# Kernel tuning notes

Measured on AMD Instinct MI355X. Metric: run time of the kernel, lower is better.

## Reference

```python
import jax, jax.numpy as jnp
import numpy as np

B, T, C = 2, 2048, 1024
E, F = 8, 1024        # n_experts, expert ffn dim
FS = 2048             # shared expert ffn dim
TOP_K = 2


def setup_inputs() -> dict:
    key = jax.random.key(0)
    ks = jax.random.split(key, 6)
    s = lambda *d: 1.0 / np.sqrt(d[-1])
    return {
        "hidden_tensor": jax.random.normal(ks[0], (B, T, C), jnp.float32),
        "w_router": jax.random.normal(ks[1], (E, C), jnp.float32) * s(C),
        "w1_stack": jax.random.normal(ks[2], (E, F, C), jnp.float32) * s(C),
        "w2_stack": jax.random.normal(ks[3], (E, C, F), jnp.float32) * s(F),
        "ws1": jax.random.normal(ks[4], (FS, C), jnp.float32) * s(C),
        "ws2": jax.random.normal(ks[5], (C, FS), jnp.float32) * s(FS),
    }


def reference(hidden_tensor, w_router, w1_stack, w2_stack, ws1, ws2):
    Bb, Tt, Cc = hidden_tensor.shape
    x = hidden_tensor.reshape(-1, Cc)                      # (t, C)
    t = x.shape[0]

    # --- router: softmax over experts, top-k, renormalize ---
    logits = x @ w_router.T                                # (t, E)
    probs = jax.nn.softmax(logits, axis=-1)
    expert_weight, expert_idx = jax.lax.top_k(probs, TOP_K)  # (t, k)
    expert_weight = expert_weight / jnp.sum(expert_weight, axis=-1, keepdims=True)

    # --- dispatch: stable sort token-expert pairs by expert id ---
    flat_e = expert_idx.reshape(-1)                        # (t*k,)
    order = jnp.argsort(flat_e, stable=True)
    sorted_e = flat_e[order]
    flat_tok = jnp.repeat(jnp.arange(t), TOP_K)
    sorted_tok = flat_tok[order]
    sorted_w = expert_weight.reshape(-1)[order]

    counts = jnp.bincount(sorted_e, length=E)              # (E,)
    offsets = jnp.concatenate([jnp.zeros((1,), counts.dtype), jnp.cumsum(counts)])
    local_pos = jnp.arange(t * TOP_K) - offsets[sorted_e]  # position within expert bin

    cap = t * TOP_K  # static capacity (>= true cnt_max), padding rows stay zero
    binned = jnp.zeros((E, cap, Cc), x.dtype).at[sorted_e, local_pos].set(x[sorted_tok])

    # --- grouped expert FFN with squared-ReLU ---
    inter = jnp.einsum('ecd,efd->ecf', binned, w1_stack)   # (E, cap, F)
    inter = jnp.square(jax.nn.relu(inter))
    outb = jnp.einsum('ecf,edf->ecd', inter, w2_stack)     # (E, cap, C)

    # --- combine: gather back, weight, scatter-add to tokens ---
    flat_out = outb[sorted_e, local_pos] * sorted_w[:, None]
    moe_out = jnp.zeros((t, Cc), x.dtype).at[sorted_tok].add(flat_out)
    moe_out = moe_out.reshape(Bb, Tt, Cc)

    # --- shared expert on residual (squared-ReLU MLP) ---
    sh = jnp.square(jax.nn.relu(jnp.einsum('btc,fc->btf', hidden_tensor, ws1)))
    shared_out = jnp.einsum('btf,cf->btc', sh, ws2)

    return shared_out + moe_out
```

## Files before the change

### kernel.cpp

```cpp
#include <hip/hip_runtime.h>
#include <math.h>

typedef unsigned short u16;
typedef unsigned int u32;

typedef __attribute__((ext_vector_type(8))) short bf16x8;
typedef __attribute__((ext_vector_type(4))) float f32x4;

__device__ __forceinline__ u16 f2bf(float f) {
  union { float f; u32 u; } v; v.f = f;
  u32 r = v.u + 0x7FFFu + ((v.u >> 16) & 1u);
  return (u16)(r >> 16);
}
__device__ __forceinline__ float bf2f(u16 h) {
  union { u32 u; float f; } v; v.u = ((u32)h) << 16; return v.f;
}

typedef const u32 __attribute__((address_space(1)))* gas1_t;
typedef u32 __attribute__((address_space(3)))* las3_t;

__device__ __forceinline__ void gload16(const void* g, void* l) {
  __builtin_amdgcn_global_load_lds((gas1_t)g, (las3_t)l, 16, 0, 0);
}

struct Tile { int kind; int g0; int n0; int e; };

__global__ __launch_bounds__(256) void prep_kernel(
    const float* __restrict__ x, const float* __restrict__ wr,
    u16* __restrict__ xb, int* __restrict__ tokE, float* __restrict__ tokW,
    const float4* __restrict__ w1, const float4* __restrict__ w2,
    const float4* __restrict__ s1, const float4* __restrict__ s2,
    ushort4* __restrict__ o1, ushort4* __restrict__ o2,
    ushort4* __restrict__ o3, ushort4* __restrict__ o4) {
  if (blockIdx.x >= 1024) {
    size_t i = (size_t)(blockIdx.x - 1024) * 256 + threadIdx.x;
    const size_t n1 = 2097152, n2 = 2097152, n3 = 524288;
    float4 v; ushort4* o; size_t j;
    if (i < n1)              { v = w1[i];            o = o1; j = i; }
    else if (i < n1+n2)      { v = w2[i-n1];         o = o2; j = i-n1; }
    else if (i < n1+n2+n3)   { v = s1[i-n1-n2];      o = o3; j = i-n1-n2; }
    else                     { v = s2[i-n1-n2-n3];   o = o4; j = i-n1-n2-n3; }
    ushort4 r; r.x = f2bf(v.x); r.y = f2bf(v.y); r.z = f2bf(v.z); r.w = f2bf(v.w);
    o[j] = r;
    return;
  }
  const int wv = threadIdx.x >> 6, lane = threadIdx.x & 63;
  const int tok = blockIdx.x * 4 + wv;
  const float4* xp = (const float4*)(x + (size_t)tok * 1024);
  float4 xv[4];
#pragma unroll
  for (int i = 0; i < 4; ++i) xv[i] = xp[i * 64 + lane];
  ushort4* xo = (ushort4*)xb + (size_t)tok * 256;
#pragma unroll
  for (int i = 0; i < 4; ++i) {
    ushort4 o;
    o.x = f2bf(xv[i].x); o.y = f2bf(xv[i].y); o.z = f2bf(xv[i].z); o.w = f2bf(xv[i].w);
    xo[i * 64 + lane] = o;
  }
  float acc[8];
#pragma unroll
  for (int e = 0; e < 8; ++e) acc[e] = 0.f;
#pragma unroll
  for (int e = 0; e < 8; ++e) {
    const float4* wp = (const float4*)(wr + e * 1024);
#pragma unroll
    for (int i = 0; i < 4; ++i) {
      float4 w4 = wp[i * 64 + lane];
      acc[e] += xv[i].x * w4.x + xv[i].y * w4.y + xv[i].z * w4.z + xv[i].w * w4.w;
    }
  }
#pragma unroll
  for (int m = 32; m > 0; m >>= 1)
#pragma unroll
    for (int e = 0; e < 8; ++e) acc[e] += __shfl_xor(acc[e], m, 64);
  if (lane == 0) {
    int e0 = 0;
#pragma unroll
    for (int e = 1; e < 8; ++e) if (acc[e] > acc[e0]) e0 = e;
    int e1 = (e0 == 0) ? 1 : 0;
#pragma unroll
    for (int e = 0; e < 8; ++e) if (e != e0 && acc[e] > acc[e1]) e1 = e;
    float p1 = __expf(acc[e1] - acc[e0]);
    float w1_ = p1 / (1.f + p1);
    float w0 = 1.f - w1_;
    tokE[tok * 2] = e0; tokE[tok * 2 + 1] = e1;
    tokW[tok * 2] = w0; tokW[tok * 2 + 1] = w1_;
  }
}

__global__ __launch_bounds__(256) void plan_kernel(
    const int* __restrict__ tokE, const float* __restrict__ tokW,
    Tile* __restrict__ upT, Tile* __restrict__ downT,
    int* __restrict__ rowtok, float* __restrict__ roww, int* __restrict__ invrow) {
  const int t = threadIdx.x, lane = t & 63, wv = t >> 6;
  int myE[32];
#pragma unroll
  for (int i = 0; i < 32; ++i) myE[i] = tokE[t * 32 + i];
  int lcnt[8] = {};
#pragma unroll
  for (int i = 0; i < 32; ++i) ++lcnt[myE[i]];

  __shared__ int wtot[8][4];
  __shared__ int aoffS[9];
  __shared__ int etile[72 * 2];
  int excl[8];
#pragma unroll
  for (int e = 0; e < 8; ++e) {
    int v = lcnt[e];
#pragma unroll
    for (int off = 1; off < 64; off <<= 1) {
      int n = __shfl_up(v, (unsigned)off, 64);
      if (lane >= off) v += n;
    }
    if (lane == 63) wtot[e][wv] = v;
    excl[e] = v - lcnt[e];
  }
  __syncthreads();
#pragma unroll
  for (int e = 0; e < 8; ++e)
    for (int w = 0; w < wv; ++w) excl[e] += wtot[e][w];

  if (t == 0) {
    int s = 0, ti = 0;
    for (int e = 0; e < 8; ++e) {
      aoffS[e] = s;
      int cnt = wtot[e][0] + wtot[e][1] + wtot[e][2] + wtot[e][3];
      int tiles = (cnt + 127) >> 7;
      for (int k = 0; k < tiles; ++k) { etile[2 * ti] = e; etile[2 * ti + 1] = s + k * 128; ++ti; }
      s += tiles << 7;
    }
    aoffS[8] = s;
    for (; ti < 72; ++ti) { etile[2 * ti] = -1; etile[2 * ti + 1] = 0; }
  }
  for (int i = t; i < 9216; i += 256) { rowtok[i] = 0; roww[i] = 0.f; }
  __syncthreads();

  for (int i = t; i < 1088; i += 256) {
    int x = i & 7, s = i >> 3;
    Tile tl;
    if (s < 64) {
      int gg = x & 3, nn = x >> 2;
      int gl = s & 7, nl = s >> 3;
      tl.kind = 0; tl.g0 = (gg * 8 + gl) * 128; tl.n0 = (nn * 8 + nl) * 128; tl.e = 0;
    } else {
      int s2_ = s - 64;
      int mg = x & 3, ng = x >> 2;
      int ml = s2_ % 18, nl = s2_ / 18;
      int mi = mg * 18 + ml;
      int e = etile[2 * mi];
      tl.kind = (e < 0) ? -1 : 1; tl.g0 = etile[2 * mi + 1];
      tl.n0 = (ng * 4 + nl) * 128; tl.e = (e < 0) ? 0 : e;
    }
    upT[i] = tl;
  }
  for (int i = t; i < 832; i += 256) {
    int x = i & 7, s = i >> 3;
    Tile tl;
    if (s < 32) {
      int gg = x & 3, nn = x >> 2;
      int gl = s & 7, nl = s >> 3;
      tl.kind = 0; tl.g0 = (gg * 8 + gl) * 128; tl.n0 = (nn * 4 + nl) * 128; tl.e = 0;
    } else {
      int s2_ = s - 32;
      int mg = x & 3, ng = x >> 2;
      int ml = s2_ % 18, nl = s2_ / 18;
      int mi = mg * 18 + ml;
      int e = etile[2 * mi];
      tl.kind = (e < 0) ? -1 : 1; tl.g0 = etile[2 * mi + 1];
      tl.n0 = (ng * 4 + nl) * 128; tl.e = (e < 0) ? 0 : e;
    }
    downT[i] = tl;
  }

  int pos[8];
#pragma unroll
  for (int e = 0; e < 8; ++e) pos[e] = aoffS[e] + excl[e];
#pragma unroll
  for (int i = 0; i < 32; ++i) {
    int idx = t * 32 + i;
    int e = myE[i];
    int g = pos[e]++;
    rowtok[g] = idx >> 1;
    roww[g] = tokW[idx];
    invrow[idx] = g;
  }
}

__global__ __launch_bounds__(256) void combine_kernel(
    const u16* __restrict__ Ym, const int* __restrict__ invrow,
    const float* __restrict__ tokW, float* __restrict__ out) {
  const int t = blockIdx.x;
  const int r0 = invrow[2 * t], r1 = invrow[2 * t + 1];
  const float w0 = tokW[2 * t], w1 = tokW[2 * t + 1];
  const ushort4* y0 = (const ushort4*)(Ym + (size_t)r0 * 1024);
  const ushort4* y1 = (const ushort4*)(Ym + (size_t)r1 * 1024);
  float4* o = (float4*)(out + (size_t)t * 1024);
  const int c = threadIdx.x;
  ushort4 a = y0[c], b = y1[c];
  float4 v = o[c];
  v.x += w0 * bf2f(a.x) + w1 * bf2f(b.x);
  v.y += w0 * bf2f(a.y) + w1 * bf2f(b.y);
  v.z += w0 * bf2f(a.z) + w1 * bf2f(b.z);
  v.w += w0 * bf2f(a.w) + w1 * bf2f(b.w);
  o[c] = v;
}

template <int PHASE>
__global__ __launch_bounds__(256)
void gemm_fused(const Tile* __restrict__ tiles,
                const u16* __restrict__ A0, const u16* __restrict__ B0, void* __restrict__ C0,
                const u16* __restrict__ A1, const u16* __restrict__ B1, void* __restrict__ C1,
                const int* __restrict__ rowtok, const float* __restrict__ roww) {
  __shared__ u16 As[128 * 64];
  __shared__ u16 Bs[128 * 64];

  Tile tm = tiles[blockIdx.x];
  if (tm.kind < 0) return;
  if (PHASE == 2 && tm.kind != 0) return;
  if (PHASE == 3 && tm.kind != 1) return;

  const int tid = threadIdx.x;
  const int lane = tid & 63;
  const int wv = tid >> 6;
  const int wrow = wv >> 1, wcol = wv & 1;

  const u16* A; const u16* B; void* C; int N, K;
  if (tm.kind == 0) {
    A = A0; B = B0; C = C0;
    N = (PHASE == 0) ? 2048 : 1024;
    K = (PHASE == 0) ? 1024 : 2048;
  } else {
    A = A1; B = B1 + ((size_t)tm.e << 20); C = (PHASE == 3) ? C0 : C1;
    N = 1024; K = 1024;
  }
  const int g0 = tm.g0, n0 = tm.n0;

  const u16* aSrc[4];
  const u16* bSrc[4];
#pragma unroll
  for (int p = 0; p < 4; ++p) {
    int c = p * 256 + tid;
    int row = c >> 3;
    int q = ((c & 7) - row) & 7;
    int arow = g0 + row;
    if (PHASE == 0 && tm.kind == 1) arow = rowtok[arow];
    aSrc[p] = A + (size_t)arow * K + q * 8;
    bSrc[p] = B + (size_t)(n0 + row) * K + q * 8;
  }
  const u32 ldsW = (u32)(wv * 64) * 16u;

  const int fr = lane & 15, fq = lane >> 4;
  const int sw0 = ((fq + fr) & 7) * 8;
  const int sw1 = ((fq + 4 + fr) & 7) * 8;
  const int aRow = (wrow * 64 + fr) * 64;
  const int bRow = (wcol * 64 + fr) * 64;

  f32x4 acc[4][4] = {};

  for (int k0 = 0; k0 < K; k0 += 64) {
#pragma unroll
    for (int p = 0; p < 4; ++p) {
      gload16(aSrc[p] + k0, (char*)As + ldsW + p * 4096);
      gload16(bSrc[p] + k0, (char*)Bs + ldsW + p * 4096);
    }
    __syncthreads();
#pragma unroll
    for (int ks = 0; ks < 2; ++ks) {
      const int sw = ks ? sw1 : sw0;
      bf16x8 af[4], bfg[4];
#pragma unroll
      for (int i = 0; i < 4; ++i) af[i] = *(const bf16x8*)&As[aRow + i * 1024 + sw];
#pragma unroll
      for (int j = 0; j < 4; ++j) bfg[j] = *(const bf16x8*)&Bs[bRow + j * 1024 + sw];
#pragma unroll
      for (int i = 0; i < 4; ++i)
#pragma unroll
        for (int j = 0; j < 4; ++j)
          acc[i][j] = __builtin_amdgcn_mfma_f32_16x16x32_bf16(af[i], bfg[j], acc[i][j], 0, 0, 0);
    }
    __syncthreads();
  }

  if (PHASE == 0) {
    u16* O = (u16*)C;
#pragma unroll
    for (int i = 0; i < 4; ++i) {
      int rb = g0 + wrow * 64 + i * 16 + fq * 4;
#pragma unroll
      for (int j = 0; j < 4; ++j) {
        int col = n0 + wcol * 64 + j * 16 + fr;
#pragma unroll
        for (int r = 0; r < 4; ++r) {
          float v = acc[i][j][r];
          v = v > 0.f ? v * v : 0.f;
          O[(size_t)(rb + r) * N + col] = f2bf(v);
        }
      }
    }
  } else if (PHASE == 1) {
    if (tm.kind == 0) {
      float* O = (float*)C;
#pragma unroll
      for (int i = 0; i < 4; ++i) {
        int rb = g0 + wrow * 64 + i * 16 + fq * 4;
#pragma unroll
        for (int j = 0; j < 4; ++j) {
          int col = n0 + wcol * 64 + j * 16 + fr;
#pragma unroll
          for (int r = 0; r < 4; ++r)
            O[(size_t)(rb + r) * N + col] = acc[i][j][r];
        }
      }
    } else {
      u16* O = (u16*)C;
#pragma unroll
      for (int i = 0; i < 4; ++i) {
        int rb = g0 + wrow * 64 + i * 16 + fq * 4;
#pragma unroll
        for (int j = 0; j < 4; ++j) {
          int col = n0 + wcol * 64 + j * 16 + fr;
#pragma unroll
          for (int r = 0; r < 4; ++r)
            O[(size_t)(rb + r) * N + col] = f2bf(acc[i][j][r]);
        }
      }
    }
  } else if (PHASE == 2) {
    float* O = (float*)C;
#pragma unroll
    for (int i = 0; i < 4; ++i) {
      int rb = g0 + wrow * 64 + i * 16 + fq * 4;
#pragma unroll
      for (int j = 0; j < 4; ++j) {
        int col = n0 + wcol * 64 + j * 16 + fr;
#pragma unroll
        for (int r = 0; r < 4; ++r)
          O[(size_t)(rb + r) * N + col] = acc[i][j][r];
      }
    }
  } else {
    float* O = (float*)C;
#pragma unroll
    for (int i = 0; i < 4; ++i) {
      int rb = g0 + wrow * 64 + i * 16 + fq * 4;
#pragma unroll
      for (int r = 0; r < 4; ++r) {
        int tok = rowtok[rb + r];
        float w = roww[rb + r];
#pragma unroll
        for (int j = 0; j < 4; ++j) {
          int col = n0 + wcol * 64 + j * 16 + fr;
          atomicAdd(&O[(size_t)tok * N + col], w * acc[i][j][r]);
        }
      }
    }
  }
}

extern "C" void kernel_launch(void* const* d_in, const int* in_sizes, int n_in,
                              void* d_out, int out_size, void* d_ws, size_t ws_size,
                              hipStream_t stream) {
  const float* x   = (const float*)d_in[0];
  const float* wr  = (const float*)d_in[1];
  const float* w1  = (const float*)d_in[2];
  const float* w2  = (const float*)d_in[3];
  const float* s1  = (const float*)d_in[4];
  const float* s2  = (const float*)d_in[5];
  float* out = (float*)d_out;

  char* p = (char*)d_ws;
  auto alloc = [&](size_t n) { char* r = p; p += (n + 255) & ~(size_t)255; return r; };
  u16* xb   = (u16*)alloc(4096ULL * 1024 * 2);
  u16* w1b  = (u16*)alloc(8ULL * 1024 * 1024 * 2);
  u16* w2b  = (u16*)alloc(8ULL * 1024 * 1024 * 2);
  u16* s1b  = (u16*)alloc(2048ULL * 1024 * 2);
  u16* s2b  = (u16*)alloc(1024ULL * 2048 * 2);
  u16* Hs   = (u16*)alloc(4096ULL * 2048 * 2);
  u16* Hm   = (u16*)alloc(9216ULL * 1024 * 2);
  int* tokE = (int*)alloc(8192 * 4);
  float* tokW = (float*)alloc(8192 * 4);
  int* rowtok = (int*)alloc(9216 * 4);
  float* roww = (float*)alloc(9216 * 4);
  int* invrow = (int*)alloc(8192 * 4);
  Tile* upT   = (Tile*)alloc(1088 * sizeof(Tile));
  Tile* downT = (Tile*)alloc(832 * sizeof(Tile));
  size_t used_base = (size_t)(p - (char*)d_ws);
  u16* Ym = (u16*)p;
  const bool haveYm = (ws_size - used_base) >= 9216ULL * 1024 * 2;

  prep_kernel<<<21504, 256, 0, stream>>>(
      x, wr, xb, tokE, tokW,
      (const float4*)w1, (const float4*)w2, (const float4*)s1, (const float4*)s2,
      (ushort4*)w1b, (ushort4*)w2b, (ushort4*)s1b, (ushort4*)s2b);

  plan_kernel<<<1, 256, 0, stream>>>(tokE, tokW, upT, downT, rowtok, roww, invrow);

  gemm_fused<0><<<1088, 256, 0, stream>>>(upT, xb, s1b, Hs, xb, w1b, Hm, rowtok, roww);

  if (haveYm) {
    gemm_fused<1><<<832, 256, 0, stream>>>(downT, Hs, s2b, out, Hm, w2b, Ym, rowtok, roww);
    combine_kernel<<<4096, 256, 0, stream>>>(Ym, invrow, tokW, out);
  } else {
    gemm_fused<2><<<832, 256, 0, stream>>>(downT, Hs, s2b, out, Hm, w2b, nullptr, rowtok, roww);
    gemm_fused<3><<<832, 256, 0, stream>>>(downT, Hs, s2b, out, Hm, w2b, nullptr, rowtok, roww);
  }
}
```

Before: 278.1 us.

## Register-prefetch GEMM tiles and move rowtok zeroing into prep kernel

The GEMM main loop no longer uses global_load_lds direct-to-LDS copies. It now loads the next K-slice into registers while MFMAs run on the current LDS tile, then stores the slice into LDS between barriers. This is meant to hide global memory latency behind compute, at the cost of extra VGPRs and a register-to-LDS store step. Separately, zeroing of rowtok/roww moves from the single-block plan kernel into extra blocks of the prep kernel, taking serial work off the one-block launch.

```diff
diff --git a/kernel.cpp b/kernel.cpp
--- a/kernel.cpp
+++ b/kernel.cpp
@@ -14,13 +14,6 @@
 }
 __device__ __forceinline__ float bf2f(u16 h) {
   union { u32 u; float f; } v; v.u = ((u32)h) << 16; return v.f;
-}
-
-typedef const u32 __attribute__((address_space(1)))* gas1_t;
-typedef u32 __attribute__((address_space(3)))* las3_t;
-
-__device__ __forceinline__ void gload16(const void* g, void* l) {
-  __builtin_amdgcn_global_load_lds((gas1_t)g, (las3_t)l, 16, 0, 0);
 }
 
 struct Tile { int kind; int g0; int n0; int e; };
@@ -31,7 +24,13 @@
     const float4* __restrict__ w1, const float4* __restrict__ w2,
     const float4* __restrict__ s1, const float4* __restrict__ s2,
     ushort4* __restrict__ o1, ushort4* __restrict__ o2,
-    ushort4* __restrict__ o3, ushort4* __restrict__ o4) {
+    ushort4* __restrict__ o3, ushort4* __restrict__ o4,
+    int* __restrict__ rowtok, float* __restrict__ roww) {
+  if (blockIdx.x >= 21504) {
+    int i = (blockIdx.x - 21504) * 256 + threadIdx.x;
+    if (i < 9216) { rowtok[i] = 0; roww[i] = 0.f; }
+    return;
+  }
   if (blockIdx.x >= 1024) {
     size_t i = (size_t)(blockIdx.x - 1024) * 256 + threadIdx.x;
     const size_t n1 = 2097152, n2 = 2097152, n3 = 524288;
@@ -132,7 +131,6 @@
     aoffS[8] = s;
     for (; ti < 72; ++ti) { etile[2 * ti] = -1; etile[2 * ti + 1] = 0; }
   }
-  for (int i = t; i < 9216; i += 256) { rowtok[i] = 0; roww[i] = 0.f; }
   __syncthreads();
 
   for (int i = t; i < 1088; i += 256) {
@@ -247,7 +245,8 @@
     aSrc[p] = A + (size_t)arow * K + q * 8;
     bSrc[p] = B + (size_t)(n0 + row) * K + q * 8;
   }
-  const u32 ldsW = (u32)(wv * 64) * 16u;
+  float4* AsV = (float4*)As;
+  float4* BsV = (float4*)Bs;
 
   const int fr = lane & 15, fq = lane >> 4;
   const int sw0 = ((fq + fr) & 7) * 8;
@@ -256,14 +255,29 @@
   const int bRow = (wcol * 64 + fr) * 64;
 
   f32x4 acc[4][4] = {};
+  float4 av[4], bv[4];
+
+#pragma unroll
+  for (int p = 0; p < 4; ++p) {
+    av[p] = *(const float4*)(aSrc[p]);
+    bv[p] = *(const float4*)(bSrc[p]);
+  }
+#pragma unroll
+  for (int p = 0; p < 4; ++p) {
+    AsV[p * 256 + tid] = av[p];
+    BsV[p * 256 + tid] = bv[p];
+  }
+  __syncthreads();
 
   for (int k0 = 0; k0 < K; k0 += 64) {
-#pragma unroll
-    for (int p = 0; p < 4; ++p) {
-      gload16(aSrc[p] + k0, (char*)As + ldsW + p * 4096);
-      gload16(bSrc[p] + k0, (char*)Bs + ldsW + p * 4096);
-    }
-    __syncthreads();
+    const bool more = (k0 + 64) < K;
+    if (more) {
+#pragma unroll
+      for (int p = 0; p < 4; ++p) {
+        av[p] = *(const float4*)(aSrc[p] + k0 + 64);
+        bv[p] = *(const float4*)(bSrc[p] + k0 + 64);
+      }
+    }
 #pragma unroll
     for (int ks = 0; ks < 2; ++ks) {
       const int sw = ks ? sw1 : sw0;
@@ -278,7 +292,15 @@
         for (int j = 0; j < 4; ++j)
           acc[i][j] = __builtin_amdgcn_mfma_f32_16x16x32_bf16(af[i], bfg[j], acc[i][j], 0, 0, 0);
     }
-    __syncthreads();
+    if (more) {
+      __syncthreads();
+#pragma unroll
+      for (int p = 0; p < 4; ++p) {
+        AsV[p * 256 + tid] = av[p];
+        BsV[p * 256 + tid] = bv[p];
+      }
+      __syncthreads();
+    }
   }
 
   if (PHASE == 0) {
@@ -388,10 +410,11 @@
   u16* Ym = (u16*)p;
   const bool haveYm = (ws_size - used_base) >= 9216ULL * 1024 * 2;
 
-  prep_kernel<<<21504, 256, 0, stream>>>(
+  prep_kernel<<<21540, 256, 0, stream>>>(
       x, wr, xb, tokE, tokW,
       (const float4*)w1, (const float4*)w2, (const float4*)s1, (const float4*)s2,
-      (ushort4*)w1b, (ushort4*)w2b, (ushort4*)s1b, (ushort4*)s2b);
+      (ushort4*)w1b, (ushort4*)w2b, (ushort4*)s1b, (ushort4*)s2b,
+      rowtok, roww);
 
   plan_kernel<<<1, 256, 0, stream>>>(tokE, tokW, upT, downT, rowtok, roww, invrow);
 
```

Result: slower. 526.0 us (+89.1%).

## Fuse down-projection and combine via atomic adds into zeroed output

Applied to the files above, without the earlier changes.

Removes the bf16 Ym intermediate and the separate combine kernel. The down-projection GEMM now atomically adds both shared-expert and weighted routed-expert results straight into the output, which is zeroed with a memset beforehand; padding rows with zero weight are skipped. The rowtok/roww zeroing moves from the single-block plan kernel into extra prep blocks, and the weight conversion now handles 8 elements per thread. In exchange every output element takes three fp32 atomic adds, which adds contention and makes the summation order nondeterministic.

```diff
diff --git a/kernel.cpp b/kernel.cpp
--- a/kernel.cpp
+++ b/kernel.cpp
@@ -5,15 +5,13 @@
 typedef unsigned int u32;
 
 typedef __attribute__((ext_vector_type(8))) short bf16x8;
+typedef __attribute__((ext_vector_type(8))) unsigned short us8;
 typedef __attribute__((ext_vector_type(4))) float f32x4;
 
 __device__ __forceinline__ u16 f2bf(float f) {
   union { float f; u32 u; } v; v.f = f;
   u32 r = v.u + 0x7FFFu + ((v.u >> 16) & 1u);
   return (u16)(r >> 16);
-}
-__device__ __forceinline__ float bf2f(u16 h) {
-  union { u32 u; float f; } v; v.u = ((u32)h) << 16; return v.f;
 }
 
 typedef const u32 __attribute__((address_space(1)))* gas1_t;
@@ -30,17 +28,26 @@
     u16* __restrict__ xb, int* __restrict__ tokE, float* __restrict__ tokW,
     const float4* __restrict__ w1, const float4* __restrict__ w2,
     const float4* __restrict__ s1, const float4* __restrict__ s2,
-    ushort4* __restrict__ o1, ushort4* __restrict__ o2,
-    ushort4* __restrict__ o3, ushort4* __restrict__ o4) {
+    us8* __restrict__ o1, us8* __restrict__ o2,
+    us8* __restrict__ o3, us8* __restrict__ o4,
+    int* __restrict__ rowtok, float* __restrict__ roww) {
+  if (blockIdx.x >= 11264) {
+    int i = (blockIdx.x - 11264) * 256 + threadIdx.x;
+    if (i < 9216) { rowtok[i] = 0; roww[i] = 0.f; }
+    return;
+  }
   if (blockIdx.x >= 1024) {
     size_t i = (size_t)(blockIdx.x - 1024) * 256 + threadIdx.x;
-    const size_t n1 = 2097152, n2 = 2097152, n3 = 524288;
-    float4 v; ushort4* o; size_t j;
-    if (i < n1)              { v = w1[i];            o = o1; j = i; }
-    else if (i < n1+n2)      { v = w2[i-n1];         o = o2; j = i-n1; }
-    else if (i < n1+n2+n3)   { v = s1[i-n1-n2];      o = o3; j = i-n1-n2; }
-    else                     { v = s2[i-n1-n2-n3];   o = o4; j = i-n1-n2-n3; }
-    ushort4 r; r.x = f2bf(v.x); r.y = f2bf(v.y); r.z = f2bf(v.z); r.w = f2bf(v.w);
+    const size_t n1 = 1048576, n2 = 1048576, n3 = 262144;
+    const float4* src; us8* o; size_t j;
+    if (i < n1)              { src = w1; o = o1; j = i; }
+    else if (i < n1+n2)      { src = w2; o = o2; j = i-n1; }
+    else if (i < n1+n2+n3)   { src = s1; o = o3; j = i-n1-n2; }
+    else                     { src = s2; o = o4; j = i-n1-n2-n3; }
+    float4 a = src[2*j], b = src[2*j+1];
+    us8 r;
+    r[0] = f2bf(a.x); r[1] = f2bf(a.y); r[2] = f2bf(a.z); r[3] = f2bf(a.w);
+    r[4] = f2bf(b.x); r[5] = f2bf(b.y); r[6] = f2bf(b.z); r[7] = f2bf(b.w);
     o[j] = r;
     return;
   }
@@ -91,7 +98,7 @@
 __global__ __launch_bounds__(256) void plan_kernel(
     const int* __restrict__ tokE, const float* __restrict__ tokW,
     Tile* __restrict__ upT, Tile* __restrict__ downT,
-    int* __restrict__ rowtok, float* __restrict__ roww, int* __restrict__ invrow) {
+    int* __restrict__ rowtok, float* __restrict__ roww) {
   const int t = threadIdx.x, lane = t & 63, wv = t >> 6;
   int myE[32];
 #pragma unroll
@@ -132,7 +139,6 @@
     aoffS[8] = s;
     for (; ti < 72; ++ti) { etile[2 * ti] = -1; etile[2 * ti + 1] = 0; }
   }
-  for (int i = t; i < 9216; i += 256) { rowtok[i] = 0; roww[i] = 0.f; }
   __syncthreads();
 
   for (int i = t; i < 1088; i += 256) {
@@ -182,27 +188,7 @@
     int g = pos[e]++;
     rowtok[g] = idx >> 1;
     roww[g] = tokW[idx];
-    invrow[idx] = g;
-  }
-}
-
-__global__ __launch_bounds__(256) void combine_kernel(
-    const u16* __restrict__ Ym, const int* __restrict__ invrow,
-    const float* __restrict__ tokW, float* __restrict__ out) {
-  const int t = blockIdx.x;
-  const int r0 = invrow[2 * t], r1 = invrow[2 * t + 1];
-  const float w0 = tokW[2 * t], w1 = tokW[2 * t + 1];
-  const ushort4* y0 = (const ushort4*)(Ym + (size_t)r0 * 1024);
-  const ushort4* y1 = (const ushort4*)(Ym + (size_t)r1 * 1024);
-  float4* o = (float4*)(out + (size_t)t * 1024);
-  const int c = threadIdx.x;
-  ushort4 a = y0[c], b = y1[c];
-  float4 v = o[c];
-  v.x += w0 * bf2f(a.x) + w1 * bf2f(b.x);
-  v.y += w0 * bf2f(a.y) + w1 * bf2f(b.y);
-  v.z += w0 * bf2f(a.z) + w1 * bf2f(b.z);
-  v.w += w0 * bf2f(a.w) + w1 * bf2f(b.w);
-  o[c] = v;
+  }
 }
 
 template <int PHASE>
@@ -216,8 +202,6 @@
 
   Tile tm = tiles[blockIdx.x];
   if (tm.kind < 0) return;
-  if (PHASE == 2 && tm.kind != 0) return;
-  if (PHASE == 3 && tm.kind != 1) return;
 
   const int tid = threadIdx.x;
   const int lane = tid & 63;
@@ -230,7 +214,7 @@
     N = (PHASE == 0) ? 2048 : 1024;
     K = (PHASE == 0) ? 1024 : 2048;
   } else {
-    A = A1; B = B1 + ((size_t)tm.e << 20); C = (PHASE == 3) ? C0 : C1;
+    A = A1; B = B1 + ((size_t)tm.e << 20); C = C1;
     N = 1024; K = 1024;
   }
   const int g0 = tm.g0, n0 = tm.n0;
@@ -297,60 +281,23 @@
         }
       }
     }
-  } else if (PHASE == 1) {
-    if (tm.kind == 0) {
-      float* O = (float*)C;
-#pragma unroll
-      for (int i = 0; i < 4; ++i) {
-        int rb = g0 + wrow * 64 + i * 16 + fq * 4;
-#pragma unroll
-        for (int j = 0; j < 4; ++j) {
-          int col = n0 + wcol * 64 + j * 16 + fr;
-#pragma unroll
-          for (int r = 0; r < 4; ++r)
-            O[(size_t)(rb + r) * N + col] = acc[i][j][r];
-        }
-      }
-    } else {
-      u16* O = (u16*)C;
-#pragma unroll
-      for (int i = 0; i < 4; ++i) {
-        int rb = g0 + wrow * 64 + i * 16 + fq * 4;
-#pragma unroll
-        for (int j = 0; j < 4; ++j) {
-          int col = n0 + wcol * 64 + j * 16 + fr;
-#pragma unroll
-          for (int r = 0; r < 4; ++r)
-            O[(size_t)(rb + r) * N + col] = f2bf(acc[i][j][r]);
-        }
-      }
-    }
-  } else if (PHASE == 2) {
+  } else {
     float* O = (float*)C;
 #pragma unroll
     for (int i = 0; i < 4; ++i) {
       int rb = g0 + wrow * 64 + i * 16 + fq * 4;
 #pragma unroll
-      for (int j = 0; j < 4; ++j) {
-        int col = n0 + wcol * 64 + j * 16 + fr;
-#pragma unroll
-        for (int r = 0; r < 4; ++r)
-          O[(size_t)(rb + r) * N + col] = acc[i][j][r];
-      }
-    }
-  } else {
-    float* O = (float*)C;
-#pragma unroll
-    for (int i = 0; i < 4; ++i) {
-      int rb = g0 + wrow * 64 + i * 16 + fq * 4;
-#pragma unroll
       for (int r = 0; r < 4; ++r) {
-        int tok = rowtok[rb + r];
-        float w = roww[rb + r];
-#pragma unroll
-        for (int j = 0; j < 4; ++j) {
-          int col = n0 + wcol * 64 + j * 16 + fr;
-          atomicAdd(&O[(size_t)tok * N + col], w * acc[i][j][r]);
+        int row = rb + r;
+        int tok; float w;
+        if (tm.kind == 0) { tok = row; w = 1.f; }
+        else { tok = rowtok[row]; w = roww[row]; }
+        if (w != 0.f) {
+#pragma unroll
+          for (int j = 0; j < 4; ++j) {
+            int col = n0 + wcol * 64 + j * 16 + fr;
+            atomicAdd(&O[(size_t)tok * 1024 + col], w * acc[i][j][r]);
+          }
         }
       }
     }
@@ -381,27 +328,20 @@
   float* tokW = (float*)alloc(8192 * 4);
   int* rowtok = (int*)alloc(9216 * 4);
   float* roww = (float*)alloc(9216 * 4);
-  int* invrow = (int*)alloc(8192 * 4);
   Tile* upT   = (Tile*)alloc(1088 * sizeof(Tile));
   Tile* downT = (Tile*)alloc(832 * sizeof(Tile));
-  size_t used_base = (size_t)(p - (char*)d_ws);
-  u16* Ym = (u16*)p;
-  const bool haveYm = (ws_size - used_base) >= 9216ULL * 1024 * 2;
-
-  prep_kernel<<<21504, 256, 0, stream>>>(
+
+  hipMemsetAsync(out, 0, (size_t)out_size * 4, stream);
+
+  prep_kernel<<<11300, 256, 0, stream>>>(
       x, wr, xb, tokE, tokW,
       (const float4*)w1, (const float4*)w2, (const float4*)s1, (const float4*)s2,
-      (ushort4*)w1b, (ushort4*)w2b, (ushort4*)s1b, (ushort4*)s2b);
-
-  plan_kernel<<<1, 256, 0, stream>>>(tokE, tokW, upT, downT, rowtok, roww, invrow);
+      (us8*)w1b, (us8*)w2b, (us8*)s1b, (us8*)s2b,
+      rowtok, roww);
+
+  plan_kernel<<<1, 256, 0, stream>>>(tokE, tokW, upT, downT, rowtok, roww);
 
   gemm_fused<0><<<1088, 256, 0, stream>>>(upT, xb, s1b, Hs, xb, w1b, Hm, rowtok, roww);
 
-  if (haveYm) {
-    gemm_fused<1><<<832, 256, 0, stream>>>(downT, Hs, s2b, out, Hm, w2b, Ym, rowtok, roww);
-    combine_kernel<<<4096, 256, 0, stream>>>(Ym, invrow, tokW, out);
-  } else {
-    gemm_fused<2><<<832, 256, 0, stream>>>(downT, Hs, s2b, out, Hm, w2b, nullptr, rowtok, roww);
-    gemm_fused<3><<<832, 256, 0, stream>>>(downT, Hs, s2b, out, Hm, w2b, nullptr, rowtok, roww);
-  }
-}
+  gemm_fused<1><<<832, 256, 0, stream>>>(downT, Hs, s2b, out, Hm, w2b, out, rowtok, roww);
+}
```

Measured after the change: 292.7 us. +5.2%, slower.
